# Kernel optimization log

Hardware: AMD Instinct MI355X
Metric: run time of the kernel (lower is better)

## Reference

```python
import jax, jax.numpy as jnp
import numpy as np

EPS = 1e-5

def conv1x1(x, w, b):
    # x: [B,C,H,W], w: [O,C], b: [O] -> [B,O,H,W]
    return jnp.einsum('bchw,oc->bohw', x, w) + b[None, :, None, None]

def batchnorm(x, gamma, beta):
    # training-mode BN over (N,H,W) with biased variance, matching torch forward
    mean = jnp.mean(x, axis=(0, 2, 3), keepdims=True)
    var = jnp.var(x, axis=(0, 2, 3), keepdims=True)
    xhat = (x - mean) * jax.lax.rsqrt(var + EPS)
    return xhat * gamma[None, :, None, None] + beta[None, :, None, None]

def setup_inputs() -> dict:
    key = jax.random.key(0)
    ks = jax.random.split(key, 16)
    B, C, F_int, H, W = 16, 256, 128, 64, 64
    s = 0.05
    return {
        'g': jax.random.normal(ks[0], (B, C, H, W), jnp.float32),
        'x': jax.random.normal(ks[1], (B, C, H, W), jnp.float32),
        'wg_w': jax.random.normal(ks[2], (F_int, C), jnp.float32) * s,
        'wg_b': jax.random.normal(ks[3], (F_int,), jnp.float32) * s,
        'wg_gamma': jnp.ones((F_int,), jnp.float32),
        'wg_beta': jnp.zeros((F_int,), jnp.float32),
        'wx_w': jax.random.normal(ks[4], (F_int, C), jnp.float32) * s,
        'wx_b': jax.random.normal(ks[5], (F_int,), jnp.float32) * s,
        'wx_gamma': jnp.ones((F_int,), jnp.float32),
        'wx_beta': jnp.zeros((F_int,), jnp.float32),
        'psi_w': jax.random.normal(ks[6], (1, F_int), jnp.float32) * s,
        'psi_b': jax.random.normal(ks[7], (1,), jnp.float32) * s,
        'psi_gamma': jnp.ones((1,), jnp.float32),
        'psi_beta': jnp.zeros((1,), jnp.float32),
    }

def reference(g, x, wg_w, wg_b, wg_gamma, wg_beta,
              wx_w, wx_b, wx_gamma, wx_beta,
              psi_w, psi_b, psi_gamma, psi_beta):
    g1 = batchnorm(conv1x1(g, wg_w, wg_b), wg_gamma, wg_beta)
    x1 = batchnorm(conv1x1(x, wx_w, wx_b), wx_gamma, wx_beta)
    psi = jax.nn.relu(g1 + x1)
    psi = jax.nn.sigmoid(batchnorm(conv1x1(psi, psi_w, psi_b), psi_gamma, psi_beta))
    return x * psi
```

## Files before the change

kernel.cpp:

```cpp
#include <hip/hip_runtime.h>
#include <hip/hip_bf16.h>
#include <math.h>

#define Bn 16
#define Cc 256
#define Oo 128
#define HWn 4096
#define Ntot 65536
#define BK 64

typedef __attribute__((ext_vector_type(8))) __bf16 bf16x8;
typedef __attribute__((ext_vector_type(4))) float f32x4;

__device__ __forceinline__ unsigned short f2bf(float f) {
    unsigned u = __builtin_bit_cast(unsigned, f);
    u = (u + 0x7FFFu + ((u >> 16) & 1u)) >> 16;
    return (unsigned short)u;
}

__device__ __forceinline__ float bf2f(unsigned short h) {
    return __builtin_bit_cast(float, (unsigned)h << 16);
}

__global__ __launch_bounds__(256, 2)
void conv_mfma(const float* __restrict__ gin, const float* __restrict__ xin,
               const float* __restrict__ wgw, const float* __restrict__ wxw,
               unsigned short* __restrict__ tg, unsigned short* __restrict__ tx,
               float* __restrict__ pstat)
{
    const int z = blockIdx.z;
    const float* in = z ? xin : gin;
    const float* w  = z ? wxw : wgw;
    unsigned short* out = z ? tx : tg;

    __shared__ short A_s[128][72];
    __shared__ unsigned int B_s[32][129];

    const int t    = threadIdx.x;
    const int b    = blockIdx.y;
    const int hw0  = blockIdx.x * 128;
    const int lane = t & 63;
    const int wv   = t >> 6;
    const int m0   = (wv & 1) * 64;
    const int n0   = (wv >> 1) * 64;
    const int q    = lane >> 4;
    const int r    = lane & 15;

    const int su  = t & 31;
    const int sc2 = t >> 5;
    const int au  = t & 15;
    const int ao  = t >> 4;

    f32x4 acc[4][4];
#pragma unroll
    for (int i = 0; i < 4; i++)
#pragma unroll
        for (int j = 0; j < 4; j++) acc[i][j] = (f32x4){0.f, 0.f, 0.f, 0.f};

    float4 bv[8];
    float4 av[8];
    auto issue = [&](int kc) {
#pragma unroll
        for (int i = 0; i < 4; i++) {
            const int c = kc + (sc2 + i * 8) * 2;
            bv[2 * i + 0] = *(const float4*)(in + (b * Cc + c) * HWn + hw0 + su * 4);
            bv[2 * i + 1] = *(const float4*)(in + (b * Cc + c + 1) * HWn + hw0 + su * 4);
        }
#pragma unroll
        for (int i = 0; i < 8; i++)
            av[i] = *(const float4*)(w + (ao + i * 16) * Cc + kc + au * 4);
    };

    issue(0);

    for (int kc = 0; kc < Cc; kc += BK) {
#pragma unroll
        for (int i = 0; i < 4; i++) {
            const int c2 = sc2 + i * 8;
            const float4 v0 = bv[2 * i + 0];
            const float4 v1 = bv[2 * i + 1];
            uint4 pk;
            pk.x = (unsigned)f2bf(v0.x) | ((unsigned)f2bf(v1.x) << 16);
            pk.y = (unsigned)f2bf(v0.y) | ((unsigned)f2bf(v1.y) << 16);
            pk.z = (unsigned)f2bf(v0.z) | ((unsigned)f2bf(v1.z) << 16);
            pk.w = (unsigned)f2bf(v0.w) | ((unsigned)f2bf(v1.w) << 16);
            *(uint4*)&B_s[c2][su * 4] = pk;
        }
#pragma unroll
        for (int i = 0; i < 8; i++) {
            const int o = ao + i * 16;
            const float4 v = av[i];
            unsigned int lo = (unsigned)f2bf(v.x) | ((unsigned)f2bf(v.y) << 16);
            unsigned int hi = (unsigned)f2bf(v.z) | ((unsigned)f2bf(v.w) << 16);
            *(uint2*)&A_s[o][au * 4] = make_uint2(lo, hi);
        }
        __syncthreads();

        if (kc + BK < Cc) issue(kc + BK);

#pragma unroll
        for (int ks = 0; ks < 2; ks++) {
            bf16x8 af[4];
#pragma unroll
            for (int mi = 0; mi < 4; mi++)
                af[mi] = *(const bf16x8*)&A_s[m0 + mi * 16 + r][ks * 32 + q * 8];
#pragma unroll
            for (int ni = 0; ni < 4; ni++) {
                unsigned int bw[4];
                const int nn = n0 + ni * 16 + r;
                const int row = ks * 16 + q * 4;
#pragma unroll
                for (int jj = 0; jj < 4; jj++) bw[jj] = B_s[row + jj][nn];
                const bf16x8 bfr = *(const bf16x8*)bw;
#pragma unroll
                for (int mi = 0; mi < 4; mi++)
                    acc[mi][ni] = __builtin_amdgcn_mfma_f32_16x16x32_bf16(af[mi], bfr, acc[mi][ni], 0, 0, 0);
            }
        }
        __syncthreads();
    }

    float* red = (float*)&A_s[0][0];
    const int hf = wv >> 1;
#pragma unroll
    for (int mi = 0; mi < 4; mi++) {
#pragma unroll
        for (int reg = 0; reg < 4; reg++) {
            const int o = m0 + mi * 16 + q * 4 + reg;
            float s1 = 0.f, s2 = 0.f;
#pragma unroll
            for (int ni = 0; ni < 4; ni++) {
                const float v = acc[mi][ni][reg];
                out[((b * Oo + o) << 12) + hw0 + n0 + ni * 16 + r] = f2bf(v);
                s1 += v; s2 += v * v;
            }
#pragma unroll
            for (int d = 1; d < 16; d <<= 1) {
                s1 += __shfl_xor(s1, d);
                s2 += __shfl_xor(s2, d);
            }
            if (r == 0) {
                red[(hf * 2 + 0) * 128 + o] = s1;
                red[(hf * 2 + 1) * 128 + o] = s2;
            }
        }
    }
    __syncthreads();
    {
        const int o = t & 127;
        const int s = t >> 7;
        const float v = red[(0 + s) * 128 + o] + red[(2 + s) * 128 + o];
        const int blk = blockIdx.y * 32 + blockIdx.x;
        pstat[(size_t)(((((z << 7) | o) << 1) | s) << 9) | blk] = v;
    }
}

__global__ void finalize1(const float* __restrict__ pstat,
                          const float* __restrict__ wg_gamma, const float* __restrict__ wg_beta,
                          const float* __restrict__ wx_gamma, const float* __restrict__ wx_beta,
                          const float* __restrict__ psi_w, float4* __restrict__ coef)
{
    const int o = blockIdx.x;
    const int t = threadIdx.x;
    const float* r00 = pstat + (size_t)(((0 * 128 + o) * 2 + 0)) * 512;
    const float* r01 = pstat + (size_t)(((0 * 128 + o) * 2 + 1)) * 512;
    const float* r10 = pstat + (size_t)(((1 * 128 + o) * 2 + 0)) * 512;
    const float* r11 = pstat + (size_t)(((1 * 128 + o) * 2 + 1)) * 512;
    float s1g = r00[t] + r00[t + 256];
    float s2g = r01[t] + r01[t + 256];
    float s1x = r10[t] + r10[t + 256];
    float s2x = r11[t] + r11[t + 256];
#pragma unroll
    for (int d = 1; d < 64; d <<= 1) {
        s1g += __shfl_xor(s1g, d);
        s2g += __shfl_xor(s2g, d);
        s1x += __shfl_xor(s1x, d);
        s2x += __shfl_xor(s2x, d);
    }
    __shared__ float rr[4][4];
    const int wv = t >> 6, lid = t & 63;
    if (lid == 0) { rr[0][wv] = s1g; rr[1][wv] = s2g; rr[2][wv] = s1x; rr[3][wv] = s2x; }
    __syncthreads();
    if (t == 0) {
        const float invN = 1.f / (float)Ntot;
        const float S1g = rr[0][0] + rr[0][1] + rr[0][2] + rr[0][3];
        const float S2g = rr[1][0] + rr[1][1] + rr[1][2] + rr[1][3];
        const float S1x = rr[2][0] + rr[2][1] + rr[2][2] + rr[2][3];
        const float S2x = rr[3][0] + rr[3][1] + rr[3][2] + rr[3][3];
        const float mg = S1g * invN;
        const float vg = S2g * invN - mg * mg;
        const float gs = wg_gamma[o] * rsqrtf(vg + 1e-5f);
        const float gh = wg_beta[o] - mg * gs;
        const float mx = S1x * invN;
        const float vx = S2x * invN - mx * mx;
        const float xs = wx_gamma[o] * rsqrtf(vx + 1e-5f);
        const float xh = wx_beta[o] - mx * xs;
        coef[o] = make_float4(gs, xs, gh + xh, psi_w[o]);
    }
}

__global__ __launch_bounds__(256)
void psi_k(const unsigned short* __restrict__ tg, const unsigned short* __restrict__ tx,
           const float4* __restrict__ coef, float* __restrict__ S, float* __restrict__ pp)
{
    __shared__ float4 cf[128];
    const int t = threadIdx.x;
    if (t < 128) cf[t] = coef[t];
    __syncthreads();

    const int p  = blockIdx.x * 256 + t;
    const int b  = p >> 12;
    const int hw = p & 4095;
    const unsigned short* gp = tg + (((size_t)(b * Oo)) << 12) + hw;
    const unsigned short* xp = tx + (((size_t)(b * Oo)) << 12) + hw;
    float s = 0.f;
#pragma unroll 16
    for (int o = 0; o < 128; o++) {
        const float gv = bf2f(gp[(size_t)o << 12]);
        const float xv = bf2f(xp[(size_t)o << 12]);
        const float4 c = cf[o];
        s += c.w * fmaxf(c.x * gv + c.y * xv + c.z, 0.f);
    }
    S[p] = s;

    float s1 = s, s2 = s * s;
#pragma unroll
    for (int d = 1; d < 64; d <<= 1) {
        s1 += __shfl_xor(s1, d);
        s2 += __shfl_xor(s2, d);
    }
    __shared__ float r1[4], r2[4];
    const int wv = t >> 6, lid = t & 63;
    if (lid == 0) { r1[wv] = s1; r2[wv] = s2; }
    __syncthreads();
    if (t == 0) {
        pp[blockIdx.x]       = r1[0] + r1[1] + r1[2] + r1[3];
        pp[256 + blockIdx.x] = r2[0] + r2[1] + r2[2] + r2[3];
    }
}

__global__ void finalize2(const float* __restrict__ pp, const float* __restrict__ psi_gamma,
                          const float* __restrict__ psi_beta, float* __restrict__ pc)
{
    const int t = threadIdx.x;
    float s1 = pp[t];
    float s2 = pp[256 + t];
#pragma unroll
    for (int d = 1; d < 64; d <<= 1) {
        s1 += __shfl_xor(s1, d);
        s2 += __shfl_xor(s2, d);
    }
    __shared__ float a1[4], a2[4];
    const int wid = t >> 6, lid = t & 63;
    if (lid == 0) { a1[wid] = s1; a2[wid] = s2; }
    __syncthreads();
    if (t == 0) {
        const float invN = 1.f / (float)Ntot;
        const float S1 = a1[0] + a1[1] + a1[2] + a1[3];
        const float S2 = a2[0] + a2[1] + a2[2] + a2[3];
        const float m = S1 * invN;
        const float v = S2 * invN - m * m;
        const float ps = psi_gamma[0] * rsqrtf(v + 1e-5f);
        pc[0] = ps;
        pc[1] = psi_beta[0] - m * ps;
    }
}

__global__ __launch_bounds__(256)
void final_mul_kernel(const float* __restrict__ x, const float* __restrict__ S,
                      const float* __restrict__ pc, float* __restrict__ out)
{
    const size_t i = ((size_t)blockIdx.x * 256 + threadIdx.x) * 4;
    const int hw = (int)(i & 4095);
    const size_t bc = i >> 12;
    const int b = (int)(bc >> 8);
    const float ps = pc[0], psh = pc[1];
    const float4 xv = *(const float4*)(x + i);
    const float4 sv = *(const float4*)(S + ((size_t)b << 12) + hw);
    float4 r;
    r.x = xv.x * (1.f / (1.f + __expf(-(ps * sv.x + psh))));
    r.y = xv.y * (1.f / (1.f + __expf(-(ps * sv.y + psh))));
    r.z = xv.z * (1.f / (1.f + __expf(-(ps * sv.z + psh))));
    r.w = xv.w * (1.f / (1.f + __expf(-(ps * sv.w + psh))));
    *(float4*)(out + i) = r;
}

extern "C" void kernel_launch(void* const* d_in, const int* in_sizes, int n_in,
                              void* d_out, int out_size, void* d_ws, size_t ws_size,
                              hipStream_t stream)
{
    const float* g         = (const float*)d_in[0];
    const float* x         = (const float*)d_in[1];
    const float* wg_w      = (const float*)d_in[2];
    const float* wg_gamma  = (const float*)d_in[4];
    const float* wg_beta   = (const float*)d_in[5];
    const float* wx_w      = (const float*)d_in[6];
    const float* wx_gamma  = (const float*)d_in[8];
    const float* wx_beta   = (const float*)d_in[9];
    const float* psi_w     = (const float*)d_in[10];
    const float* psi_gamma = (const float*)d_in[12];
    const float* psi_beta  = (const float*)d_in[13];

    float* out = (float*)d_out;
    unsigned short* tg = (unsigned short*)out;
    unsigned short* tx = (unsigned short*)out + (size_t)Bn * Oo * HWn;

    float* ws    = (float*)d_ws;
    float* S     = ws;
    float* pstat = ws + 65536;
    float4* coef = (float4*)(ws + 327680);
    float* pp    = ws + 327680 + 512;
    float* pc    = ws + 328704;


    conv_mfma<<<dim3(HWn / 128, Bn, 2), 256, 0, stream>>>(
        g, x, wg_w, wx_w, tg, tx, pstat);
    finalize1<<<128, 256, 0, stream>>>(pstat, wg_gamma, wg_beta, wx_gamma, wx_beta,
                                       psi_w, coef);
    psi_k<<<256, 256, 0, stream>>>(tg, tx, coef, S, pp);
    finalize2<<<1, 256, 0, stream>>>(pp, psi_gamma, psi_beta, pc);
    final_mul_kernel<<<(Ntot * Cc) / (4 * 256), 256, 0, stream>>>(x, S, pc, out);
}
```

Before: 257.2 us.

## Fuse pipeline into one persistent kernel with grid barriers and register-resident activations

Replaces the five-kernel pipeline with a single persistent kernel of 512 blocks. Each block computes both 1x1 convs for its tile and keeps the accumulators in registers. Grid-wide atomic barriers separate the BN statistics reduction from the psi computation and the final sigmoid multiply. This removes the bf16 intermediate round trips through global memory and several launches, but it relies on all 512 blocks being co-resident, doubles accumulator register pressure, and makes the stats reduction order nondeterministic through float atomics.

```diff
diff --git a/kernel.cpp b/kernel.cpp
--- a/kernel.cpp
+++ b/kernel.cpp
@@ -8,6 +8,7 @@
 #define HWn 4096
 #define Ntot 65536
 #define BK 64
+#define GRID 512
 
 typedef __attribute__((ext_vector_type(8))) __bf16 bf16x8;
 typedef __attribute__((ext_vector_type(4))) float f32x4;
@@ -18,27 +19,30 @@
     return (unsigned short)u;
 }
 
-__device__ __forceinline__ float bf2f(unsigned short h) {
-    return __builtin_bit_cast(float, (unsigned)h << 16);
-}
-
 __global__ __launch_bounds__(256, 2)
-void conv_mfma(const float* __restrict__ gin, const float* __restrict__ xin,
-               const float* __restrict__ wgw, const float* __restrict__ wxw,
-               unsigned short* __restrict__ tg, unsigned short* __restrict__ tx,
-               float* __restrict__ pstat)
+void fused(const float* __restrict__ gin, const float* __restrict__ xin,
+           const float* __restrict__ wgw, const float* __restrict__ wxw,
+           const float* __restrict__ wg_gamma, const float* __restrict__ wg_beta,
+           const float* __restrict__ wx_gamma, const float* __restrict__ wx_beta,
+           const float* __restrict__ psi_w, const float* __restrict__ psi_gamma,
+           const float* __restrict__ psi_beta,
+           float* __restrict__ outp,
+           float* __restrict__ gstat,
+           float* __restrict__ psum,
+           unsigned* __restrict__ bar)
 {
-    const int z = blockIdx.z;
-    const float* in = z ? xin : gin;
-    const float* w  = z ? wxw : wgw;
-    unsigned short* out = z ? tx : tg;
-
     __shared__ short A_s[128][72];
     __shared__ unsigned int B_s[32][129];
+    __shared__ float red[8][129];
+    __shared__ float sfin[128];
+    __shared__ float lgs[128], lxs[128], lch[128], lpw[128];
+    __shared__ float rr[4];
+    __shared__ float pcl[2];
 
     const int t    = threadIdx.x;
-    const int b    = blockIdx.y;
-    const int hw0  = blockIdx.x * 128;
+    const int bid  = blockIdx.x;
+    const int b    = bid >> 5;
+    const int hw0  = (bid & 31) * 128;
     const int lane = t & 63;
     const int wv   = t >> 6;
     const int m0   = (wv & 1) * 64;
@@ -51,15 +55,18 @@
     const int au  = t & 15;
     const int ao  = t >> 4;
 
-    f32x4 acc[4][4];
+    f32x4 accg[4][4], accx[4][4];
 #pragma unroll
     for (int i = 0; i < 4; i++)
 #pragma unroll
-        for (int j = 0; j < 4; j++) acc[i][j] = (f32x4){0.f, 0.f, 0.f, 0.f};
+        for (int j = 0; j < 4; j++) {
+            accg[i][j] = (f32x4){0.f, 0.f, 0.f, 0.f};
+            accx[i][j] = (f32x4){0.f, 0.f, 0.f, 0.f};
+        }
 
     float4 bv[8];
     float4 av[8];
-    auto issue = [&](int kc) {
+    auto issue = [&](const float* in, const float* w, int kc) {
 #pragma unroll
         for (int i = 0; i < 4; i++) {
             const int c = kc + (sc2 + i * 8) * 2;
@@ -71,9 +78,7 @@
             av[i] = *(const float4*)(w + (ao + i * 16) * Cc + kc + au * 4);
     };
 
-    issue(0);
-
-    for (int kc = 0; kc < Cc; kc += BK) {
+    auto stage_convert = [&]() {
 #pragma unroll
         for (int i = 0; i < 4; i++) {
             const int c2 = sc2 + i * 8;
@@ -94,10 +99,9 @@
             unsigned int hi = (unsigned)f2bf(v.z) | ((unsigned)f2bf(v.w) << 16);
             *(uint2*)&A_s[o][au * 4] = make_uint2(lo, hi);
         }
-        __syncthreads();
-
-        if (kc + BK < Cc) issue(kc + BK);
-
+    };
+
+    auto do_mfma = [&](f32x4 (&acc)[4][4]) {
 #pragma unroll
         for (int ks = 0; ks < 2; ks++) {
             bf16x8 af[4];
@@ -117,172 +121,169 @@
                     acc[mi][ni] = __builtin_amdgcn_mfma_f32_16x16x32_bf16(af[mi], bfr, acc[mi][ni], 0, 0, 0);
             }
         }
-        __syncthreads();
-    }
-
-    float* red = (float*)&A_s[0][0];
+    };
+
+    auto gridbar = [&](unsigned* c) {
+        __syncthreads();
+        if (t == 0) {
+            __threadfence();
+            __hip_atomic_fetch_add(c, 1u, __ATOMIC_ACQ_REL, __HIP_MEMORY_SCOPE_AGENT);
+            long guard = 0;
+            while (__hip_atomic_load(c, __ATOMIC_ACQUIRE, __HIP_MEMORY_SCOPE_AGENT) < GRID) {
+                __builtin_amdgcn_s_sleep(8);
+                if (++guard > (1L << 25)) break;
+            }
+        }
+        __syncthreads();
+        __threadfence();
+    };
+
+    issue(gin, wgw, 0);
+    for (int kc = 0; kc < Cc; kc += BK) {
+        stage_convert();
+        __syncthreads();
+        if (kc + BK < Cc) issue(gin, wgw, kc + BK);
+        else              issue(xin, wxw, 0);
+        do_mfma(accg);
+        __syncthreads();
+    }
+    for (int kc = 0; kc < Cc; kc += BK) {
+        stage_convert();
+        __syncthreads();
+        if (kc + BK < Cc) issue(xin, wxw, kc + BK);
+        do_mfma(accx);
+        __syncthreads();
+    }
+
     const int hf = wv >> 1;
-#pragma unroll
-    for (int mi = 0; mi < 4; mi++) {
+    auto stats_half = [&](f32x4 (&acc)[4][4], int z) {
+#pragma unroll
+        for (int mi = 0; mi < 4; mi++)
+#pragma unroll
+            for (int reg = 0; reg < 4; reg++) {
+                const int o = m0 + mi * 16 + q * 4 + reg;
+                float s1 = 0.f, s2 = 0.f;
+#pragma unroll
+                for (int ni = 0; ni < 4; ni++) {
+                    const float v = acc[mi][ni][reg];
+                    s1 += v; s2 += v * v;
+                }
+#pragma unroll
+                for (int d = 1; d < 16; d <<= 1) {
+                    s1 += __shfl_xor(s1, d);
+                    s2 += __shfl_xor(s2, d);
+                }
+                if (r == 0) {
+                    red[z * 4 + hf * 2 + 0][o] = s1;
+                    red[z * 4 + hf * 2 + 1][o] = s2;
+                }
+            }
+    };
+    stats_half(accg, 0);
+    stats_half(accx, 1);
+    __syncthreads();
+    for (int e = t; e < 512; e += 256) {
+        const int zz = e >> 8, s = (e >> 7) & 1, o = e & 127;
+        const float v = red[zz * 4 + s][o] + red[zz * 4 + 2 + s][o];
+        atomicAdd(&gstat[(((zz << 7) | o) << 1) | s], v);
+    }
+
+    gridbar(&bar[0]);
+
+    if (t < 128) {
+        const float s1g = __hip_atomic_load(&gstat[(t << 1) | 0], __ATOMIC_RELAXED, __HIP_MEMORY_SCOPE_AGENT);
+        const float s2g = __hip_atomic_load(&gstat[(t << 1) | 1], __ATOMIC_RELAXED, __HIP_MEMORY_SCOPE_AGENT);
+        const float s1x = __hip_atomic_load(&gstat[256 + ((t << 1) | 0)], __ATOMIC_RELAXED, __HIP_MEMORY_SCOPE_AGENT);
+        const float s2x = __hip_atomic_load(&gstat[256 + ((t << 1) | 1)], __ATOMIC_RELAXED, __HIP_MEMORY_SCOPE_AGENT);
+        const float invN = 1.f / (float)Ntot;
+        const float mg = s1g * invN;
+        const float vg = s2g * invN - mg * mg;
+        const float gs = wg_gamma[t] * rsqrtf(vg + 1e-5f);
+        const float gh = wg_beta[t] - mg * gs;
+        const float mx = s1x * invN;
+        const float vx = s2x * invN - mx * mx;
+        const float xs = wx_gamma[t] * rsqrtf(vx + 1e-5f);
+        const float xh = wx_beta[t] - mx * xs;
+        lgs[t] = gs;
+        lxs[t] = xs;
+        lch[t] = gh + xh;
+        lpw[t] = psi_w[t];
+    }
+    __syncthreads();
+
+    float part[4] = {0.f, 0.f, 0.f, 0.f};
+#pragma unroll
+    for (int mi = 0; mi < 4; mi++)
 #pragma unroll
         for (int reg = 0; reg < 4; reg++) {
             const int o = m0 + mi * 16 + q * 4 + reg;
-            float s1 = 0.f, s2 = 0.f;
-#pragma unroll
-            for (int ni = 0; ni < 4; ni++) {
-                const float v = acc[mi][ni][reg];
-                out[((b * Oo + o) << 12) + hw0 + n0 + ni * 16 + r] = f2bf(v);
-                s1 += v; s2 += v * v;
-            }
-#pragma unroll
-            for (int d = 1; d < 16; d <<= 1) {
-                s1 += __shfl_xor(s1, d);
-                s2 += __shfl_xor(s2, d);
-            }
-            if (r == 0) {
-                red[(hf * 2 + 0) * 128 + o] = s1;
-                red[(hf * 2 + 1) * 128 + o] = s2;
-            }
-        }
-    }
-    __syncthreads();
-    {
-        const int o = t & 127;
-        const int s = t >> 7;
-        const float v = red[(0 + s) * 128 + o] + red[(2 + s) * 128 + o];
-        const int blk = blockIdx.y * 32 + blockIdx.x;
-        pstat[(size_t)(((((z << 7) | o) << 1) | s) << 9) | blk] = v;
-    }
-}
-
-__global__ void finalize1(const float* __restrict__ pstat,
-                          const float* __restrict__ wg_gamma, const float* __restrict__ wg_beta,
-                          const float* __restrict__ wx_gamma, const float* __restrict__ wx_beta,
-                          const float* __restrict__ psi_w, float4* __restrict__ coef)
-{
-    const int o = blockIdx.x;
-    const int t = threadIdx.x;
-    const float* r00 = pstat + (size_t)(((0 * 128 + o) * 2 + 0)) * 512;
-    const float* r01 = pstat + (size_t)(((0 * 128 + o) * 2 + 1)) * 512;
-    const float* r10 = pstat + (size_t)(((1 * 128 + o) * 2 + 0)) * 512;
-    const float* r11 = pstat + (size_t)(((1 * 128 + o) * 2 + 1)) * 512;
-    float s1g = r00[t] + r00[t + 256];
-    float s2g = r01[t] + r01[t + 256];
-    float s1x = r10[t] + r10[t + 256];
-    float s2x = r11[t] + r11[t + 256];
+            const float gs = lgs[o], xs = lxs[o], ch = lch[o], pw = lpw[o];
+#pragma unroll
+            for (int ni = 0; ni < 4; ni++)
+                part[ni] += pw * fmaxf(gs * accg[mi][ni][reg] + xs * accx[mi][ni][reg] + ch, 0.f);
+        }
+    const int gidx = (wv & 1) * 4 + q;
+#pragma unroll
+    for (int ni = 0; ni < 4; ni++)
+        red[gidx][n0 + ni * 16 + r] = part[ni];
+    __syncthreads();
+
+    float ps1 = 0.f, ps2 = 0.f;
+    if (t < 128) {
+        float s = 0.f;
+#pragma unroll
+        for (int gI = 0; gI < 8; gI++) s += red[gI][t];
+        sfin[t] = s;
+        ps1 = s; ps2 = s * s;
+    }
 #pragma unroll
     for (int d = 1; d < 64; d <<= 1) {
-        s1g += __shfl_xor(s1g, d);
-        s2g += __shfl_xor(s2g, d);
-        s1x += __shfl_xor(s1x, d);
-        s2x += __shfl_xor(s2x, d);
-    }
-    __shared__ float rr[4][4];
-    const int wv = t >> 6, lid = t & 63;
-    if (lid == 0) { rr[0][wv] = s1g; rr[1][wv] = s2g; rr[2][wv] = s1x; rr[3][wv] = s2x; }
+        ps1 += __shfl_xor(ps1, d);
+        ps2 += __shfl_xor(ps2, d);
+    }
+    __syncthreads();
+    if (t < 128 && lane == 0) { rr[wv] = ps1; rr[2 + wv] = ps2; }
     __syncthreads();
     if (t == 0) {
+        atomicAdd(&psum[0], rr[0] + rr[1]);
+        atomicAdd(&psum[1], rr[2] + rr[3]);
+    }
+
+    gridbar(&bar[1]);
+
+    if (t == 0) {
+        const float S1 = __hip_atomic_load(&psum[0], __ATOMIC_RELAXED, __HIP_MEMORY_SCOPE_AGENT);
+        const float S2 = __hip_atomic_load(&psum[1], __ATOMIC_RELAXED, __HIP_MEMORY_SCOPE_AGENT);
         const float invN = 1.f / (float)Ntot;
-        const float S1g = rr[0][0] + rr[0][1] + rr[0][2] + rr[0][3];
-        const float S2g = rr[1][0] + rr[1][1] + rr[1][2] + rr[1][3];
-        const float S1x = rr[2][0] + rr[2][1] + rr[2][2] + rr[2][3];
-        const float S2x = rr[3][0] + rr[3][1] + rr[3][2] + rr[3][3];
-        const float mg = S1g * invN;
-        const float vg = S2g * invN - mg * mg;
-        const float gs = wg_gamma[o] * rsqrtf(vg + 1e-5f);
-        const float gh = wg_beta[o] - mg * gs;
-        const float mx = S1x * invN;
-        const float vx = S2x * invN - mx * mx;
-        const float xs = wx_gamma[o] * rsqrtf(vx + 1e-5f);
-        const float xh = wx_beta[o] - mx * xs;
-        coef[o] = make_float4(gs, xs, gh + xh, psi_w[o]);
-    }
-}
-
-__global__ __launch_bounds__(256)
-void psi_k(const unsigned short* __restrict__ tg, const unsigned short* __restrict__ tx,
-           const float4* __restrict__ coef, float* __restrict__ S, float* __restrict__ pp)
-{
-    __shared__ float4 cf[128];
-    const int t = threadIdx.x;
-    if (t < 128) cf[t] = coef[t];
-    __syncthreads();
-
-    const int p  = blockIdx.x * 256 + t;
-    const int b  = p >> 12;
-    const int hw = p & 4095;
-    const unsigned short* gp = tg + (((size_t)(b * Oo)) << 12) + hw;
-    const unsigned short* xp = tx + (((size_t)(b * Oo)) << 12) + hw;
-    float s = 0.f;
-#pragma unroll 16
-    for (int o = 0; o < 128; o++) {
-        const float gv = bf2f(gp[(size_t)o << 12]);
-        const float xv = bf2f(xp[(size_t)o << 12]);
-        const float4 c = cf[o];
-        s += c.w * fmaxf(c.x * gv + c.y * xv + c.z, 0.f);
-    }
-    S[p] = s;
-
-    float s1 = s, s2 = s * s;
-#pragma unroll
-    for (int d = 1; d < 64; d <<= 1) {
-        s1 += __shfl_xor(s1, d);
-        s2 += __shfl_xor(s2, d);
-    }
-    __shared__ float r1[4], r2[4];
-    const int wv = t >> 6, lid = t & 63;
-    if (lid == 0) { r1[wv] = s1; r2[wv] = s2; }
-    __syncthreads();
-    if (t == 0) {
-        pp[blockIdx.x]       = r1[0] + r1[1] + r1[2] + r1[3];
-        pp[256 + blockIdx.x] = r2[0] + r2[1] + r2[2] + r2[3];
-    }
-}
-
-__global__ void finalize2(const float* __restrict__ pp, const float* __restrict__ psi_gamma,
-                          const float* __restrict__ psi_beta, float* __restrict__ pc)
-{
-    const int t = threadIdx.x;
-    float s1 = pp[t];
-    float s2 = pp[256 + t];
-#pragma unroll
-    for (int d = 1; d < 64; d <<= 1) {
-        s1 += __shfl_xor(s1, d);
-        s2 += __shfl_xor(s2, d);
-    }
-    __shared__ float a1[4], a2[4];
-    const int wid = t >> 6, lid = t & 63;
-    if (lid == 0) { a1[wid] = s1; a2[wid] = s2; }
-    __syncthreads();
-    if (t == 0) {
-        const float invN = 1.f / (float)Ntot;
-        const float S1 = a1[0] + a1[1] + a1[2] + a1[3];
-        const float S2 = a2[0] + a2[1] + a2[2] + a2[3];
         const float m = S1 * invN;
         const float v = S2 * invN - m * m;
-        const float ps = psi_gamma[0] * rsqrtf(v + 1e-5f);
-        pc[0] = ps;
-        pc[1] = psi_beta[0] - m * ps;
-    }
-}
-
-__global__ __launch_bounds__(256)
-void final_mul_kernel(const float* __restrict__ x, const float* __restrict__ S,
-                      const float* __restrict__ pc, float* __restrict__ out)
-{
-    const size_t i = ((size_t)blockIdx.x * 256 + threadIdx.x) * 4;
-    const int hw = (int)(i & 4095);
-    const size_t bc = i >> 12;
-    const int b = (int)(bc >> 8);
-    const float ps = pc[0], psh = pc[1];
-    const float4 xv = *(const float4*)(x + i);
-    const float4 sv = *(const float4*)(S + ((size_t)b << 12) + hw);
-    float4 r;
-    r.x = xv.x * (1.f / (1.f + __expf(-(ps * sv.x + psh))));
-    r.y = xv.y * (1.f / (1.f + __expf(-(ps * sv.y + psh))));
-    r.z = xv.z * (1.f / (1.f + __expf(-(ps * sv.z + psh))));
-    r.w = xv.w * (1.f / (1.f + __expf(-(ps * sv.w + psh))));
-    *(float4*)(out + i) = r;
+        const float psc = psi_gamma[0] * rsqrtf(v + 1e-5f);
+        pcl[0] = psc;
+        pcl[1] = psi_beta[0] - m * psc;
+    }
+    __syncthreads();
+
+    const float psc = pcl[0], psh = pcl[1];
+    float sig[4];
+#pragma unroll
+    for (int k = 0; k < 4; k++) {
+        const float sv = sfin[su * 4 + k];
+        sig[k] = 1.f / (1.f + __expf(-(psc * sv + psh)));
+    }
+    const float* xb = xin + (((size_t)(b * Cc)) << 12) + hw0 + su * 4;
+    float* ob = outp + (((size_t)(b * Cc)) << 12) + hw0 + su * 4;
+    const int c0 = t >> 5;
+#pragma unroll 4
+    for (int i = 0; i < 32; i++) {
+        const size_t coff = ((size_t)(c0 + i * 8)) << 12;
+        const float4 xv = *(const float4*)(xb + coff);
+        float4 rv;
+        rv.x = xv.x * sig[0];
+        rv.y = xv.y * sig[1];
+        rv.z = xv.z * sig[2];
+        rv.w = xv.w * sig[3];
+        *(float4*)(ob + coff) = rv;
+    }
 }
 
 extern "C" void kernel_launch(void* const* d_in, const int* in_sizes, int n_in,
@@ -302,22 +303,14 @@
     const float* psi_beta  = (const float*)d_in[13];
 
     float* out = (float*)d_out;
-    unsigned short* tg = (unsigned short*)out;
-    unsigned short* tx = (unsigned short*)out + (size_t)Bn * Oo * HWn;
-
-    float* ws    = (float*)d_ws;
-    float* S     = ws;
-    float* pstat = ws + 65536;
-    float4* coef = (float4*)(ws + 327680);
-    float* pp    = ws + 327680 + 512;
-    float* pc    = ws + 328704;
-
-
-    conv_mfma<<<dim3(HWn / 128, Bn, 2), 256, 0, stream>>>(
-        g, x, wg_w, wx_w, tg, tx, pstat);
-    finalize1<<<128, 256, 0, stream>>>(pstat, wg_gamma, wg_beta, wx_gamma, wx_beta,
-                                       psi_w, coef);
-    psi_k<<<256, 256, 0, stream>>>(tg, tx, coef, S, pp);
-    finalize2<<<1, 256, 0, stream>>>(pp, psi_gamma, psi_beta, pc);
-    final_mul_kernel<<<(Ntot * Cc) / (4 * 256), 256, 0, stream>>>(x, S, pc, out);
+
+    float* ws      = (float*)d_ws;
+    float* gstat   = ws;
+    float* psum    = ws + 512;
+    unsigned* bar  = (unsigned*)(ws + 514);
+    hipMemsetAsync(ws, 0, 516 * sizeof(float), stream);
+
+    fused<<<dim3(GRID), 256, 0, stream>>>(
+        g, x, wg_w, wx_w, wg_gamma, wg_beta, wx_gamma, wx_beta,
+        psi_w, psi_gamma, psi_beta, out, gstat, psum, bar);
 }
```

Result: slower. 346.1 us (+34.5%).
